# Kernel optimization log

Hardware: AMD Instinct MI355X
Metric: run time of the kernel (lower is better)

## Reference

```python
import jax, jax.numpy as jnp
import numpy as np

B, T, D, S, EXP = 4, 2048, 1024, 16, 2
E = D * EXP  # expanded channels = 2048


def setup_inputs() -> dict:
    key = jax.random.key(0)
    ks = jax.random.split(key, 8)
    s = 0.02
    f = jnp.float32
    return {
        "x": jax.random.normal(ks[0], (B, T, D), f),
        "in_w": jax.random.normal(ks[1], (2 * E, D), f) * s,
        "in_b": jnp.zeros((2 * E,), f),
        "conv_w": jax.random.normal(ks[2], (E, 1, 3), f) * s,  # depthwise conv, groups=E
        "conv_b": jnp.zeros((E,), f),
        "dt_w": jax.random.normal(ks[3], (E, E), f) * s,
        "dt_b": jnp.zeros((E,), f),
        "B_w": jax.random.normal(ks[4], (S, E), f) * s,
        "B_b": jnp.zeros((S,), f),
        "C_w": jax.random.normal(ks[5], (S, E), f) * s,
        "C_b": jnp.zeros((S,), f),
        "D_w": jax.random.normal(ks[6], (S, E), f) * s,
        "D_b": jnp.zeros((S,), f),
        "out_w": jax.random.normal(ks[7], (D, E), f) * s,
        "out_b": jnp.zeros((D,), f),
    }


def reference(x, in_w, in_b, conv_w, conv_b, dt_w, dt_b, B_w, B_b, C_w, C_b, D_w, D_b, out_w, out_b):
    silu = jax.nn.silu
    # in_proj -> split into main / gate, each [B,T,E]
    xp = x @ in_w.T + in_b
    x_main, x_gate = xp[..., :E], xp[..., E:]
    # depthwise temporal conv (kernel 3, pad 1, groups=E), then SiLU
    xc = jax.lax.conv_general_dilated(
        x_main.transpose(0, 2, 1), conv_w, (1,), [(1, 1)],
        dimension_numbers=("NCH", "OIH", "NCH"), feature_group_count=E)
    xc = silu((xc + conv_b[None, :, None]).transpose(0, 2, 1))  # [B,T,E]
    dt = jax.nn.softplus(xc @ dt_w.T + dt_b)                     # [B,T,E]
    Bt = xc @ B_w.T + B_b                                        # [B,T,S]
    Ct = xc @ C_w.T + C_b
    Dt = xc @ D_w.T + D_b
    decay = jnp.exp(jnp.clip(-dt.mean(-1), -10.0, 10.0))         # [B,T] scalar decay per step
    u = Bt * Dt                                                  # [B,T,S] state input

    def step(state, inp):  # state [B,S]
        d, u_t, c_t = inp
        state = state * d[:, None] + u_t
        return state, (c_t * state).sum(-1)  # y_t [B]

    _, ys = jax.lax.scan(step, jnp.zeros((x.shape[0], S), x.dtype),
                         (decay.T, u.transpose(1, 0, 2), Ct.transpose(1, 0, 2)))
    y = ys.T[..., None] * silu(x_gate)  # broadcast [B,T,1] -> [B,T,E] (matches .expand)
    return x + (y @ out_w.T + out_b)    # dropout in eval mode = identity
```

## Files before the change

kernel.cpp:

```cpp
#include <hip/hip_runtime.h>
#include <hip/hip_bf16.h>

#define Bsz 4
#define Tsz 2048
#define Dsz 1024
#define Ssz 16
#define Esz 2048
#define Mrows (Bsz*Tsz)

typedef __attribute__((ext_vector_type(8))) short short8;
typedef __attribute__((ext_vector_type(4))) float floatx4;
typedef __attribute__((ext_vector_type(8))) int int8v;
typedef __attribute__((ext_vector_type(4))) int int4v;

__device__ __forceinline__ void async_ld16(const void* g, void* l) {
    __builtin_amdgcn_global_load_lds(
        (const __attribute__((address_space(1))) void*)g,
        (__attribute__((address_space(3))) void*)l,
        16, 0, 0);
}

__device__ __forceinline__ float sigmoidf_(float v) { return 1.f / (1.f + expf(-v)); }
__device__ __forceinline__ float bf2f(unsigned short u) {
    union { unsigned u32; float f; } c; c.u32 = (unsigned)u << 16; return c.f;
}
__device__ __forceinline__ int pk_fp8x4(float a, float b, float c, float d) {
    int lo = __builtin_amdgcn_cvt_pk_fp8_f32(a, b, 0, 0);
    int hi = __builtin_amdgcn_cvt_pk_fp8_f32(c, d, 0, 0);
    return (lo & 0xFFFF) | (hi << 16);
}

#define WAIT_VM(N)   (0xF70 | (N))

#define CV_S0 2097152
#define CV_S1 3145728
#define CV_S2 4194304
#define CV_S3 4718592
__global__ void cvt_all(const float4* __restrict__ x,  const float4* __restrict__ iw,
                        const float4* __restrict__ dw, const float4* __restrict__ ow,
                        int* __restrict__ x8, int* __restrict__ iw8,
                        int* __restrict__ dw8, int* __restrict__ ow8) {
    int i = blockIdx.x * blockDim.x + threadIdx.x;
    const int stride = gridDim.x * blockDim.x;
    for (; i < CV_S3; i += stride) {
        if (i < CV_S0) {
            float4 v = x[i];
            x8[i] = pk_fp8x4(v.x, v.y, v.z, v.w);
        } else if (i < CV_S1) {
            const int j = i - CV_S0;
            float4 v = iw[j];
            iw8[j] = pk_fp8x4(v.x * 64.f, v.y * 64.f, v.z * 64.f, v.w * 64.f);
        } else if (i < CV_S2) {
            const int j = i - CV_S1;
            float4 v = dw[j];
            dw8[j] = pk_fp8x4(v.x * 64.f, v.y * 64.f, v.z * 64.f, v.w * 64.f);
        } else {
            const int j = i - CV_S2;
            float4 v = ow[j];
            ow8[j] = pk_fp8x4(v.x * 64.f, v.y * 64.f, v.z * 64.f, v.w * 64.f);
        }
    }
}

template<int MODE, int SA, int SB>
__launch_bounds__(256, 2)
__global__ void gemm_f8(const unsigned char* __restrict__ A,
                        const unsigned char* __restrict__ Bw,
                        const float* __restrict__ bias,
                        int M, int N, int K,
                        __hip_bfloat16* __restrict__ outb,
                        float* __restrict__ rowsum,
                        const float* __restrict__ resid,
                        const float* __restrict__ ysv,
                        float* __restrict__ outf) {
    __shared__ __align__(16) unsigned char sA[2 * 16384];
    __shared__ __align__(16) unsigned char sB[2 * 16384];

    const int tid  = threadIdx.x;
    const int wave = tid >> 6, lane = tid & 63;
    const int wm = wave >> 1, wn = wave & 1;
    const int q = lane >> 4, lr = lane & 15;

    const int gx = gridDim.x, gy = gridDim.y;
    const int flat = blockIdx.y * gx + blockIdx.x;
    const int stripe = gy >> 3;
    const int xcd = flat & 7, local = flat >> 3;
    const int mt = xcd * stripe + (local % stripe);
    const int nt = local / stripe;
    const int m0 = mt * 128, n0 = nt * 128;

    floatx4 acc[4][4];
#pragma unroll
    for (int i = 0; i < 4; ++i)
#pragma unroll
        for (int j = 0; j < 4; ++j) acc[i][j] = (floatx4){0.f, 0.f, 0.f, 0.f};

    const unsigned char* pa[4];
    const unsigned char* pb[4];
#pragma unroll
    for (int i = 0; i < 4; ++i) {
        const int idx = i * 256 + tid, row = idx >> 3, s = idx & 7;
        pa[i] = A + (size_t)(m0 + row) * K + ((s ^ (row & 7)) * 16);
        pb[i] = Bw + (size_t)(n0 + row) * K + ((s ^ (row & 7)) * 16);
    }

    const int rA = wm * 64 + lr, rB = wn * 64 + lr;
    const int oA0 = rA * 128 + (((2 * q)     ^ (rA & 7)) * 16);
    const int oA1 = rA * 128 + (((2 * q + 1) ^ (rA & 7)) * 16);
    const int oB0 = rB * 128 + (((2 * q)     ^ (rB & 7)) * 16);
    const int oB1 = rB * 128 + (((2 * q + 1) ^ (rB & 7)) * 16);

#define F8_ISSUE(ST) do {                                                      \
        _Pragma("unroll")                                                      \
        for (int i = 0; i < 4; ++i) {                                          \
            async_ld16(pa[i], &sA[(ST) * 16384 + (i * 256 + wave * 64) * 16]); \
            pa[i] += 128;                                                      \
        }                                                                      \
        _Pragma("unroll")                                                      \
        for (int i = 0; i < 4; ++i) {                                          \
            async_ld16(pb[i], &sB[(ST) * 16384 + (i * 256 + wave * 64) * 16]); \
            pb[i] += 128;                                                      \
        }                                                                      \
    } while (0)

    const int ntiles = K >> 7;
    F8_ISSUE(0);
    for (int kt = 0; kt < ntiles; ++kt) {
        const int st = kt & 1;
        __builtin_amdgcn_s_waitcnt(WAIT_VM(0));
        __syncthreads();
        F8_ISSUE(st ^ 1);

        int8v a8[4], b8[4];
#pragma unroll
        for (int i = 0; i < 4; ++i) {
            int4v lo = *(const int4v*)&sA[st * 16384 + oA0 + i * 2048];
            int4v hi = *(const int4v*)&sA[st * 16384 + oA1 + i * 2048];
            a8[i] = __builtin_shufflevector(lo, hi, 0, 1, 2, 3, 4, 5, 6, 7);
        }
#pragma unroll
        for (int j = 0; j < 4; ++j) {
            int4v lo = *(const int4v*)&sB[st * 16384 + oB0 + j * 2048];
            int4v hi = *(const int4v*)&sB[st * 16384 + oB1 + j * 2048];
            b8[j] = __builtin_shufflevector(lo, hi, 0, 1, 2, 3, 4, 5, 6, 7);
        }
#pragma unroll
        for (int i = 0; i < 4; ++i)
#pragma unroll
            for (int j = 0; j < 4; ++j)
                acc[i][j] = __builtin_amdgcn_mfma_scale_f32_16x16x128_f8f6f4(
                    a8[i], b8[j], acc[i][j], 0, 0, 0, SA, 0, SB);
    }
#undef F8_ISSUE
    __builtin_amdgcn_s_waitcnt(WAIT_VM(0));

    if (MODE == 0) {
#pragma unroll
        for (int i = 0; i < 4; ++i) {
            const int row = m0 + wm * 64 + i * 16 + q * 4;
#pragma unroll
            for (int j = 0; j < 4; ++j) {
                const int col = n0 + wn * 64 + j * 16 + lr;
                const float bc = bias[col];
#pragma unroll
                for (int r = 0; r < 4; ++r)
                    outb[(size_t)(row + r) * N + col] = __float2bfloat16(acc[i][j][r] + bc);
            }
        }
    } else if (MODE == 1) {
#pragma unroll
        for (int i = 0; i < 4; ++i) {
            float rs[4] = {0.f, 0.f, 0.f, 0.f};
#pragma unroll
            for (int j = 0; j < 4; ++j) {
                const int col = n0 + wn * 64 + j * 16 + lr;
                const float bc = bias[col];
#pragma unroll
                for (int r = 0; r < 4; ++r) {
                    float v = acc[i][j][r] + bc;
                    float sp = (v > 20.f) ? v : log1pf(expf(v));
                    rs[r] += sp;
                }
            }
#pragma unroll
            for (int r = 0; r < 4; ++r) {
                float v = rs[r];
                v += __shfl_xor(v, 1); v += __shfl_xor(v, 2);
                v += __shfl_xor(v, 4); v += __shfl_xor(v, 8);
                if (lr == 0)
                    atomicAdd(&rowsum[m0 + wm * 64 + i * 16 + q * 4 + r], v);
            }
        }
    } else {
#pragma unroll
        for (int i = 0; i < 4; ++i) {
            const int row = m0 + wm * 64 + i * 16 + q * 4;
#pragma unroll
            for (int j = 0; j < 4; ++j) {
                const int col = n0 + wn * 64 + j * 16 + lr;
                const float bc = bias[col];
#pragma unroll
                for (int r = 0; r < 4; ++r) {
                    const size_t idx = (size_t)(row + r) * N + col;
                    outf[idx] = resid[idx] + ysv[row + r] * acc[i][j][r] + bc;
                }
            }
        }
    }
}

__global__ void conv_gate_k(const __hip_bfloat16* __restrict__ xp,
                            const float* __restrict__ cw,
                            const float* __restrict__ cb,
                            __hip_bfloat16* __restrict__ xc,
                            int2* __restrict__ xc8,
                            int2* __restrict__ s8) {
    const int idx8 = blockIdx.x * blockDim.x + threadIdx.x;
    const int e = (idx8 & (Esz / 8 - 1)) * 8;
    const int r = idx8 >> 8;
    const int t = r & (Tsz - 1);
    const unsigned short* row0 = (const unsigned short*)(xp + (size_t)r * (2 * Esz) + e);
    short8 vm1 = (t > 0)       ? *(const short8*)(row0 - 2 * Esz) : (short8){0,0,0,0,0,0,0,0};
    short8 v00 = *(const short8*)row0;
    short8 vp1 = (t < Tsz - 1) ? *(const short8*)(row0 + 2 * Esz) : (short8){0,0,0,0,0,0,0,0};
    short8 o;
    float sil[8];
#pragma unroll
    for (int k = 0; k < 8; ++k) {
        const int ek = e + k;
        float v = bf2f((unsigned short)vm1[k]) * cw[ek * 3 + 0]
                + bf2f((unsigned short)v00[k]) * cw[ek * 3 + 1]
                + bf2f((unsigned short)vp1[k]) * cw[ek * 3 + 2] + cb[ek];
        sil[k] = v * sigmoidf_(v);
        __hip_bfloat16 h = __float2bfloat16(sil[k]);
        o[k] = *(short*)&h;
    }
    *(short8*)(xc + (size_t)idx8 * 8) = o;
    int2 p;
    p.x = pk_fp8x4(sil[0] * 16.f, sil[1] * 16.f, sil[2] * 16.f, sil[3] * 16.f);
    p.y = pk_fp8x4(sil[4] * 16.f, sil[5] * 16.f, sil[6] * 16.f, sil[7] * 16.f);
    xc8[idx8] = p;

    short8 g = *(const short8*)(row0 + Esz);
    float sg[8];
#pragma unroll
    for (int k = 0; k < 8; ++k) {
        const float gv = bf2f((unsigned short)g[k]);
        sg[k] = gv * sigmoidf_(gv);
    }
    int2 ps;
    ps.x = pk_fp8x4(sg[0] * 16.f, sg[1] * 16.f, sg[2] * 16.f, sg[3] * 16.f);
    ps.y = pk_fp8x4(sg[4] * 16.f, sg[5] * 16.f, sg[6] * 16.f, sg[7] * 16.f);
    s8[idx8] = ps;
}

__global__ void pack_bcd(const float* __restrict__ Bw, const float* __restrict__ Cw,
                         const float* __restrict__ Dw, __hip_bfloat16* __restrict__ Wb) {
    const int idx = blockIdx.x * blockDim.x + threadIdx.x;
    if (idx >= 48 * Esz) return;
    const int row = idx >> 11, col = idx & (Esz - 1);
    float v;
    if (row < 16)      v = Bw[row * Esz + col];
    else if (row < 32) v = Cw[(row - 16) * Esz + col];
    else               v = Dw[(row - 32) * Esz + col];
    Wb[idx] = __float2bfloat16(v);
}

__launch_bounds__(256)
__global__ void bcd_mfma(const __hip_bfloat16* __restrict__ xc,
                         const __hip_bfloat16* __restrict__ Wb,
                         const float* __restrict__ Bb, const float* __restrict__ Cb,
                         const float* __restrict__ Db,
                         float* __restrict__ u, float* __restrict__ Ct) {
    __shared__ __align__(16) __hip_bfloat16 sA[64 * 32];
    __shared__ __align__(16) __hip_bfloat16 sW[48 * 32];
    const int tid = threadIdx.x;
    const int wave = tid >> 6, lane = tid & 63;
    const int q = lane >> 4, lr = lane & 15;
    const int m0 = blockIdx.x * 64;

    floatx4 acc[3];
#pragma unroll
    for (int j = 0; j < 3; ++j) acc[j] = (floatx4){0.f, 0.f, 0.f, 0.f};

    const int ra = wave * 16 + (lane >> 2);
    const int ca = (lane & 3) * 8;

    for (int kt = 0; kt < (Esz >> 5); ++kt) {
        const int k0 = kt << 5;
        __syncthreads();
        async_ld16(&xc[(size_t)(m0 + ra) * Esz + k0 + ca], &sA[wave * 512]);
        if (wave < 3)
            async_ld16(&Wb[(size_t)ra * Esz + k0 + ca], &sW[wave * 512]);
        __syncthreads();

        short8 af = *(const short8*)&sA[(wave * 16 + lr) * 32 + q * 8];
#pragma unroll
        for (int j = 0; j < 3; ++j) {
            short8 wf = *(const short8*)&sW[(j * 16 + lr) * 32 + q * 8];
            acc[j] = __builtin_amdgcn_mfma_f32_16x16x32_bf16(af, wf, acc[j], 0, 0, 0);
        }
    }

    const int row = m0 + wave * 16 + q * 4;
    const float bb = Bb[lr], cbv = Cb[lr], db = Db[lr];
#pragma unroll
    for (int r = 0; r < 4; ++r) {
        const float bt = acc[0][r] + bb;
        const float ct = acc[1][r] + cbv;
        const float dt = acc[2][r] + db;
        u [(size_t)(row + r) * Ssz + lr] = bt * dt;
        Ct[(size_t)(row + r) * Ssz + lr] = ct;
    }
}

__global__ void scan_k(const float* __restrict__ rowsum, const float* __restrict__ u,
                       const float* __restrict__ Ct, float* __restrict__ ys) {
    const int b = blockIdx.x;
    const int tid = threadIdx.x;
    const int lane = tid & 63, wave = tid >> 6;
    __shared__ __align__(16) float su[256 * Ssz];
    __shared__ __align__(16) float sc[256 * Ssz];
    __shared__ float sp[256 * 17];
    __shared__ float sd[256];
    float st = 0.f;
    for (int t0 = 0; t0 < Tsz; t0 += 256) {
        __syncthreads();
        const float4* ub = (const float4*)(u  + ((size_t)b * Tsz + t0) * Ssz);
        const float4* cb = (const float4*)(Ct + ((size_t)b * Tsz + t0) * Ssz);
#pragma unroll
        for (int i = 0; i < 4; ++i) {
            ((float4*)su)[tid + i * 256] = ub[tid + i * 256];
            ((float4*)sc)[tid + i * 256] = cb[tid + i * 256];
        }
        {
            const float m = rowsum[b * Tsz + t0 + tid] * (1.f / (float)Esz);
            sd[tid] = expf(fminf(fmaxf(-m, -10.f), 10.f));
        }
        __syncthreads();
        if (wave == 0 && lane < 16) {
#pragma unroll 8
            for (int i = 0; i < 256; ++i) {
                st = st * sd[i] + su[i * Ssz + lane];
                sp[i * 17 + lane] = sc[i * Ssz + lane] * st;
            }
        }
        __syncthreads();
        float s = 0.f;
#pragma unroll
        for (int j = 0; j < 16; ++j) s += sp[tid * 17 + j];
        ys[b * Tsz + t0 + tid] = s;
    }
}

extern "C" void kernel_launch(void* const* d_in, const int* in_sizes, int n_in,
                              void* d_out, int out_size, void* d_ws, size_t ws_size,
                              hipStream_t stream) {
    const float* x      = (const float*)d_in[0];
    const float* in_w   = (const float*)d_in[1];
    const float* in_b   = (const float*)d_in[2];
    const float* conv_w = (const float*)d_in[3];
    const float* conv_b = (const float*)d_in[4];
    const float* dt_w   = (const float*)d_in[5];
    const float* dt_b   = (const float*)d_in[6];
    const float* B_w    = (const float*)d_in[7];
    const float* B_b    = (const float*)d_in[8];
    const float* C_w    = (const float*)d_in[9];
    const float* C_b    = (const float*)d_in[10];
    const float* D_w    = (const float*)d_in[11];
    const float* D_b    = (const float*)d_in[12];
    const float* out_w  = (const float*)d_in[13];
    const float* out_b  = (const float*)d_in[14];
    float* out = (float*)d_out;

    char* ws = (char*)d_ws;
    auto alloc = [&](size_t bytes) {
        char* p = ws;
        ws += (bytes + 255) & ~(size_t)255;
        return p;
    };
    unsigned char* x_f8    = (unsigned char*)alloc((size_t)Mrows * Dsz);
    unsigned char* inw_f8  = (unsigned char*)alloc((size_t)2 * Esz * Dsz);
    unsigned char* dtw_f8  = (unsigned char*)alloc((size_t)Esz * Esz);
    unsigned char* outw_f8 = (unsigned char*)alloc((size_t)Dsz * Esz);
    __hip_bfloat16* xp_bf  = (__hip_bfloat16*)alloc((size_t)Mrows * 2 * Esz * 2);
    __hip_bfloat16* xc_bf  = (__hip_bfloat16*)alloc((size_t)Mrows * Esz * 2);
    unsigned char* xc_f8   = (unsigned char*)alloc((size_t)Mrows * Esz);
    unsigned char* s_f8    = (unsigned char*)alloc((size_t)Mrows * Esz);
    __hip_bfloat16* wb_bf  = (__hip_bfloat16*)alloc((size_t)48 * Esz * 2);
    float* rowsum = (float*)alloc(Mrows * 4);
    float* u_buf  = (float*)alloc((size_t)Mrows * Ssz * 4);
    float* ct_buf = (float*)alloc((size_t)Mrows * Ssz * 4);
    float* ys_buf = (float*)alloc(Mrows * 4);
    (void)alloc(65536);

    hipMemsetAsync(rowsum, 0, Mrows * 4, stream);

    cvt_all<<<4608, 256, 0, stream>>>((const float4*)x, (const float4*)in_w,
                                      (const float4*)dt_w, (const float4*)out_w,
                                      (int*)x_f8, (int*)inw_f8, (int*)dtw_f8,
                                      (int*)outw_f8);
    pack_bcd<<<48 * Esz / 256, 256, 0, stream>>>(B_w, C_w, D_w, wb_bf);

    gemm_f8<0, 127, 121><<<dim3(4096 / 128, Mrows / 128), 256, 0, stream>>>(
        x_f8, inw_f8, in_b, Mrows, 4096, 1024, xp_bf, nullptr, nullptr, nullptr, nullptr);

    conv_gate_k<<<(Mrows * Esz / 8) / 256, 256, 0, stream>>>(
        xp_bf, conv_w, conv_b, xc_bf, (int2*)xc_f8, (int2*)s_f8);

    gemm_f8<1, 123, 121><<<dim3(Esz / 128, Mrows / 128), 256, 0, stream>>>(
        xc_f8, dtw_f8, dt_b, Mrows, Esz, Esz, nullptr, rowsum, nullptr, nullptr, nullptr);

    bcd_mfma<<<Mrows / 64, 256, 0, stream>>>(xc_bf, wb_bf, B_b, C_b, D_b, u_buf, ct_buf);

    scan_k<<<Bsz, 256, 0, stream>>>(rowsum, u_buf, ct_buf, ys_buf);

    gemm_f8<2, 123, 121><<<dim3(Dsz / 128, Mrows / 128), 256, 0, stream>>>(
        s_f8, outw_f8, out_b, Mrows, Dsz, Esz, nullptr, nullptr, x, ys_buf, out);
}
```

Baseline: 442.3 us.

## Use 256x256 tile FP8 GEMM with split-phase prefetch for in_proj and dt GEMMs

Adds a 512-thread GEMM kernel with 256x256 output tiles, 8 waves, and compile-time K/N for the in_proj and dt projections. Its K loop interleaves the async global-to-LDS loads of the next tile with the MFMA work, using partial waitcnts, split barriers and s_setprio. The larger tile is meant to raise arithmetic intensity and cut global and L2 traffic per flop. The cost is 128KB of LDS per block, more accumulator registers, and fewer blocks than compute units (512 and 256), which risks poor occupancy and tail imbalance. The out_proj GEMM stays on the 128x128 kernel.

```diff
diff --git a/kernel.cpp b/kernel.cpp
--- a/kernel.cpp
+++ b/kernel.cpp
@@ -62,17 +62,189 @@
     }
 }
 
-template<int MODE, int SA, int SB>
-__launch_bounds__(256, 2)
-__global__ void gemm_f8(const unsigned char* __restrict__ A,
+template<int MODE, int SA, int SB, int K, int N>
+__launch_bounds__(512, 2)
+__global__ void gemm256(const unsigned char* __restrict__ A,
                         const unsigned char* __restrict__ Bw,
                         const float* __restrict__ bias,
-                        int M, int N, int K,
                         __hip_bfloat16* __restrict__ outb,
-                        float* __restrict__ rowsum,
-                        const float* __restrict__ resid,
-                        const float* __restrict__ ysv,
-                        float* __restrict__ outf) {
+                        float* __restrict__ rowsum) {
+    __shared__ __align__(16) unsigned char sA[2 * 32768];
+    __shared__ __align__(16) unsigned char sB[2 * 32768];
+
+    const int tid  = threadIdx.x;
+    const int wave = tid >> 6, lane = tid & 63;
+    const int wm = wave >> 2, wn = wave & 3;
+    const int q = lane >> 4, lr = lane & 15;
+
+    const int gx = gridDim.x;
+    const int flat = blockIdx.y * gx + blockIdx.x;
+    const int xcd = flat & 7, local = flat >> 3;
+    const int mt = xcd * 4 + (local & 3);
+    const int nt = local >> 2;
+    const int m0 = mt * 256, n0 = nt * 256;
+
+    floatx4 acc[8][4];
+#pragma unroll
+    for (int i = 0; i < 8; ++i)
+#pragma unroll
+        for (int j = 0; j < 4; ++j) acc[i][j] = (floatx4){0.f, 0.f, 0.f, 0.f};
+
+    const int rowin = lane >> 3;
+    const int chunk = (lane & 7) ^ rowin;
+    const unsigned char* pa = A  + (size_t)(m0 + wave * 8 + rowin) * K + chunk * 16;
+    const unsigned char* pb = Bw + (size_t)(n0 + wave * 8 + rowin) * K + chunk * 16;
+    const int ldsw = wave * 8 * 128;
+
+    const int c0 = ((2 * q)     ^ (lr & 7)) * 16;
+    const int c1 = ((2 * q + 1) ^ (lr & 7)) * 16;
+    const int oA = (wm * 128 + lr) * 128;
+    const int oB = (wn * 64  + lr) * 128;
+
+#define G256_ISSUE_B(r) async_ld16(pb + (size_t)(r) * 64 * K + koff, \
+                                   &sB[sbo + ((r) * 64 * 128) + ldsw])
+#define G256_ISSUE_A(r) async_ld16(pa + (size_t)(r) * 64 * K + koff, \
+                                   &sA[sbo + ((r) * 64 * 128) + ldsw])
+#define G256_RD(dst, base, off) do {                                        \
+        int4v lo_ = *(const int4v*)&(base)[(off) + c0];                     \
+        int4v hi_ = *(const int4v*)&(base)[(off) + c1];                     \
+        dst = __builtin_shufflevector(lo_, hi_, 0, 1, 2, 3, 4, 5, 6, 7);    \
+    } while (0)
+
+    {
+        const size_t koff = 0; const int sbo = 0;
+        G256_ISSUE_B(0); G256_ISSUE_B(1); G256_ISSUE_B(2); G256_ISSUE_B(3);
+        G256_ISSUE_A(0); G256_ISSUE_A(2); G256_ISSUE_A(1); G256_ISSUE_A(3);
+    }
+
+    const int NT = K >> 7;
+    for (int kt = 0; kt < NT; ++kt) {
+        const int sb  = (kt & 1) * 32768;
+        const int sbo = ((kt + 1) & 1) * 32768;
+        const size_t koff = (size_t)(kt + 1) * 128;
+
+        __builtin_amdgcn_s_waitcnt(WAIT_VM(2));
+        __builtin_amdgcn_s_barrier();
+        G256_ISSUE_B(0); G256_ISSUE_B(1);
+        int8v b8[4];
+#pragma unroll
+        for (int g = 0; g < 4; ++g) G256_RD(b8[g], &sB[sb], oB + g * 2048);
+        {
+            int8v a0, a1;
+            G256_RD(a0, &sA[sb], oA + 0 * 2048);
+            G256_RD(a1, &sA[sb], oA + 1 * 2048);
+            __builtin_amdgcn_s_setprio(1);
+#pragma unroll
+            for (int g = 0; g < 4; ++g) {
+                acc[0][g] = __builtin_amdgcn_mfma_scale_f32_16x16x128_f8f6f4(
+                    a0, b8[g], acc[0][g], 0, 0, 0, SA, 0, SB);
+                acc[1][g] = __builtin_amdgcn_mfma_scale_f32_16x16x128_f8f6f4(
+                    a1, b8[g], acc[1][g], 0, 0, 0, SA, 0, SB);
+            }
+            __builtin_amdgcn_s_setprio(0);
+        }
+        G256_ISSUE_B(2); G256_ISSUE_B(3);
+        {
+            int8v a0, a1;
+            G256_RD(a0, &sA[sb], oA + 2 * 2048);
+            G256_RD(a1, &sA[sb], oA + 3 * 2048);
+            __builtin_amdgcn_s_setprio(1);
+#pragma unroll
+            for (int g = 0; g < 4; ++g) {
+                acc[2][g] = __builtin_amdgcn_mfma_scale_f32_16x16x128_f8f6f4(
+                    a0, b8[g], acc[2][g], 0, 0, 0, SA, 0, SB);
+                acc[3][g] = __builtin_amdgcn_mfma_scale_f32_16x16x128_f8f6f4(
+                    a1, b8[g], acc[3][g], 0, 0, 0, SA, 0, SB);
+            }
+            __builtin_amdgcn_s_setprio(0);
+        }
+        __builtin_amdgcn_s_waitcnt(WAIT_VM(4));
+        __builtin_amdgcn_s_barrier();
+        G256_ISSUE_A(0); G256_ISSUE_A(2);
+        {
+            int8v a0, a1;
+            G256_RD(a0, &sA[sb], oA + 4 * 2048);
+            G256_RD(a1, &sA[sb], oA + 5 * 2048);
+            __builtin_amdgcn_s_setprio(1);
+#pragma unroll
+            for (int g = 0; g < 4; ++g) {
+                acc[4][g] = __builtin_amdgcn_mfma_scale_f32_16x16x128_f8f6f4(
+                    a0, b8[g], acc[4][g], 0, 0, 0, SA, 0, SB);
+                acc[5][g] = __builtin_amdgcn_mfma_scale_f32_16x16x128_f8f6f4(
+                    a1, b8[g], acc[5][g], 0, 0, 0, SA, 0, SB);
+            }
+            __builtin_amdgcn_s_setprio(0);
+        }
+        G256_ISSUE_A(1); G256_ISSUE_A(3);
+        {
+            int8v a0, a1;
+            G256_RD(a0, &sA[sb], oA + 6 * 2048);
+            G256_RD(a1, &sA[sb], oA + 7 * 2048);
+            __builtin_amdgcn_s_setprio(1);
+#pragma unroll
+            for (int g = 0; g < 4; ++g) {
+                acc[6][g] = __builtin_amdgcn_mfma_scale_f32_16x16x128_f8f6f4(
+                    a0, b8[g], acc[6][g], 0, 0, 0, SA, 0, SB);
+                acc[7][g] = __builtin_amdgcn_mfma_scale_f32_16x16x128_f8f6f4(
+                    a1, b8[g], acc[7][g], 0, 0, 0, SA, 0, SB);
+            }
+            __builtin_amdgcn_s_setprio(0);
+        }
+    }
+#undef G256_ISSUE_B
+#undef G256_ISSUE_A
+#undef G256_RD
+    __builtin_amdgcn_s_waitcnt(WAIT_VM(0));
+
+    if (MODE == 0) {
+#pragma unroll
+        for (int i = 0; i < 8; ++i) {
+            const int row = m0 + wm * 128 + i * 16 + q * 4;
+#pragma unroll
+            for (int j = 0; j < 4; ++j) {
+                const int col = n0 + wn * 64 + j * 16 + lr;
+                const float bc = bias[col];
+#pragma unroll
+                for (int r = 0; r < 4; ++r)
+                    outb[(size_t)(row + r) * N + col] = __float2bfloat16(acc[i][j][r] + bc);
+            }
+        }
+    } else {
+#pragma unroll
+        for (int i = 0; i < 8; ++i) {
+            float rs[4] = {0.f, 0.f, 0.f, 0.f};
+#pragma unroll
+            for (int j = 0; j < 4; ++j) {
+                const int col = n0 + wn * 64 + j * 16 + lr;
+                const float bc = bias[col];
+#pragma unroll
+                for (int r = 0; r < 4; ++r) {
+                    float v = acc[i][j][r] + bc;
+                    float sp = (v > 20.f) ? v : log1pf(expf(v));
+                    rs[r] += sp;
+                }
+            }
+#pragma unroll
+            for (int r = 0; r < 4; ++r) {
+                float v = rs[r];
+                v += __shfl_xor(v, 1); v += __shfl_xor(v, 2);
+                v += __shfl_xor(v, 4); v += __shfl_xor(v, 8);
+                if (lr == 0)
+                    atomicAdd(&rowsum[m0 + wm * 128 + i * 16 + q * 4 + r], v);
+            }
+        }
+    }
+}
+
+template<int SA, int SB>
+__launch_bounds__(256, 2)
+__global__ void gemm_f8_sm(const unsigned char* __restrict__ A,
+                           const unsigned char* __restrict__ Bw,
+                           const float* __restrict__ bias,
+                           int M, int N, int K,
+                           const float* __restrict__ resid,
+                           const float* __restrict__ ysv,
+                           float* __restrict__ outf) {
     __shared__ __align__(16) unsigned char sA[2 * 16384];
     __shared__ __align__(16) unsigned char sB[2 * 16384];
 
@@ -123,9 +295,9 @@
         }                                                                      \
     } while (0)
 
-    const int ntiles = K >> 7;
+    const int ntile = K >> 7;
     F8_ISSUE(0);
-    for (int kt = 0; kt < ntiles; ++kt) {
+    for (int kt = 0; kt < ntile; ++kt) {
         const int st = kt & 1;
         __builtin_amdgcn_s_waitcnt(WAIT_VM(0));
         __syncthreads();
@@ -154,56 +326,17 @@
 #undef F8_ISSUE
     __builtin_amdgcn_s_waitcnt(WAIT_VM(0));
 
-    if (MODE == 0) {
-#pragma unroll
-        for (int i = 0; i < 4; ++i) {
-            const int row = m0 + wm * 64 + i * 16 + q * 4;
-#pragma unroll
-            for (int j = 0; j < 4; ++j) {
-                const int col = n0 + wn * 64 + j * 16 + lr;
-                const float bc = bias[col];
-#pragma unroll
-                for (int r = 0; r < 4; ++r)
-                    outb[(size_t)(row + r) * N + col] = __float2bfloat16(acc[i][j][r] + bc);
-            }
-        }
-    } else if (MODE == 1) {
-#pragma unroll
-        for (int i = 0; i < 4; ++i) {
-            float rs[4] = {0.f, 0.f, 0.f, 0.f};
-#pragma unroll
-            for (int j = 0; j < 4; ++j) {
-                const int col = n0 + wn * 64 + j * 16 + lr;
-                const float bc = bias[col];
-#pragma unroll
-                for (int r = 0; r < 4; ++r) {
-                    float v = acc[i][j][r] + bc;
-                    float sp = (v > 20.f) ? v : log1pf(expf(v));
-                    rs[r] += sp;
-                }
-            }
+#pragma unroll
+    for (int i = 0; i < 4; ++i) {
+        const int row = m0 + wm * 64 + i * 16 + q * 4;
+#pragma unroll
+        for (int j = 0; j < 4; ++j) {
+            const int col = n0 + wn * 64 + j * 16 + lr;
+            const float bc = bias[col];
 #pragma unroll
             for (int r = 0; r < 4; ++r) {
-                float v = rs[r];
-                v += __shfl_xor(v, 1); v += __shfl_xor(v, 2);
-                v += __shfl_xor(v, 4); v += __shfl_xor(v, 8);
-                if (lr == 0)
-                    atomicAdd(&rowsum[m0 + wm * 64 + i * 16 + q * 4 + r], v);
-            }
-        }
-    } else {
-#pragma unroll
-        for (int i = 0; i < 4; ++i) {
-            const int row = m0 + wm * 64 + i * 16 + q * 4;
-#pragma unroll
-            for (int j = 0; j < 4; ++j) {
-                const int col = n0 + wn * 64 + j * 16 + lr;
-                const float bc = bias[col];
-#pragma unroll
-                for (int r = 0; r < 4; ++r) {
-                    const size_t idx = (size_t)(row + r) * N + col;
-                    outf[idx] = resid[idx] + ysv[row + r] * acc[i][j][r] + bc;
-                }
+                const size_t idx = (size_t)(row + r) * N + col;
+                outf[idx] = resid[idx] + ysv[row + r] * acc[i][j][r] + bc;
             }
         }
     }
@@ -392,7 +525,7 @@
     float* u_buf  = (float*)alloc((size_t)Mrows * Ssz * 4);
     float* ct_buf = (float*)alloc((size_t)Mrows * Ssz * 4);
     float* ys_buf = (float*)alloc(Mrows * 4);
-    (void)alloc(65536);
+    (void)alloc(131072);
 
     hipMemsetAsync(rowsum, 0, Mrows * 4, stream);
 
@@ -402,19 +535,19 @@
                                       (int*)outw_f8);
     pack_bcd<<<48 * Esz / 256, 256, 0, stream>>>(B_w, C_w, D_w, wb_bf);
 
-    gemm_f8<0, 127, 121><<<dim3(4096 / 128, Mrows / 128), 256, 0, stream>>>(
-        x_f8, inw_f8, in_b, Mrows, 4096, 1024, xp_bf, nullptr, nullptr, nullptr, nullptr);
+    gemm256<0, 127, 121, 1024, 4096><<<dim3(16, 32), 512, 0, stream>>>(
+        x_f8, inw_f8, in_b, xp_bf, nullptr);
 
     conv_gate_k<<<(Mrows * Esz / 8) / 256, 256, 0, stream>>>(
         xp_bf, conv_w, conv_b, xc_bf, (int2*)xc_f8, (int2*)s_f8);
 
-    gemm_f8<1, 123, 121><<<dim3(Esz / 128, Mrows / 128), 256, 0, stream>>>(
-        xc_f8, dtw_f8, dt_b, Mrows, Esz, Esz, nullptr, rowsum, nullptr, nullptr, nullptr);
+    gemm256<1, 123, 121, 2048, 2048><<<dim3(8, 32), 512, 0, stream>>>(
+        xc_f8, dtw_f8, dt_b, nullptr, rowsum);
 
     bcd_mfma<<<Mrows / 64, 256, 0, stream>>>(xc_bf, wb_bf, B_b, C_b, D_b, u_buf, ct_buf);
 
     scan_k<<<Bsz, 256, 0, stream>>>(rowsum, u_buf, ct_buf, ys_buf);
 
-    gemm_f8<2, 123, 121><<<dim3(Dsz / 128, Mrows / 128), 256, 0, stream>>>(
-        s_f8, outw_f8, out_b, Mrows, Dsz, Esz, nullptr, nullptr, x, ys_buf, out);
-}
+    gemm_f8_sm<123, 121><<<dim3(Dsz / 128, Mrows / 128), 256, 0, stream>>>(
+        s_f8, outw_f8, out_b, Mrows, Dsz, Esz, x, ys_buf, out);
+}
```

New measurement: 447.4 us. About the same (+1.2%).

## Switch GEMM pipeline from scaled FP8 MFMA to BF16 MFMA

Applied to the files above, without the earlier changes.

Replaces the FP8 scaled 16x16x128 MFMA GEMMs with BF16 16x16x32 MFMA GEMMs, converting inputs, weights and the conv/gate activations to bf16 instead of fp8. K tiles shrink to 32 elements with 8 KB LDS stages, the XOR swizzle is dropped, and launch bounds rise to 3 blocks per CU. This likely aims at accuracy or simplicity, but it doubles the bytes moved and quarters the K per MFMA. It also risks LDS bank conflicts from the unswizzled layout.

```diff
diff --git a/kernel.cpp b/kernel.cpp
--- a/kernel.cpp
+++ b/kernel.cpp
@@ -10,8 +10,7 @@
 
 typedef __attribute__((ext_vector_type(8))) short short8;
 typedef __attribute__((ext_vector_type(4))) float floatx4;
-typedef __attribute__((ext_vector_type(8))) int int8v;
-typedef __attribute__((ext_vector_type(4))) int int4v;
+typedef __attribute__((ext_vector_type(4))) unsigned short ushort4v;
 
 __device__ __forceinline__ void async_ld16(const void* g, void* l) {
     __builtin_amdgcn_global_load_lds(
@@ -24,10 +23,9 @@
 __device__ __forceinline__ float bf2f(unsigned short u) {
     union { unsigned u32; float f; } c; c.u32 = (unsigned)u << 16; return c.f;
 }
-__device__ __forceinline__ int pk_fp8x4(float a, float b, float c, float d) {
-    int lo = __builtin_amdgcn_cvt_pk_fp8_f32(a, b, 0, 0);
-    int hi = __builtin_amdgcn_cvt_pk_fp8_f32(c, d, 0, 0);
-    return (lo & 0xFFFF) | (hi << 16);
+__device__ __forceinline__ unsigned short f2bf(float f) {
+    __hip_bfloat16 h = __float2bfloat16(f);
+    return *(unsigned short*)&h;
 }
 
 #define WAIT_VM(N)   (0xF70 | (N))
@@ -38,33 +36,25 @@
 #define CV_S3 4718592
 __global__ void cvt_all(const float4* __restrict__ x,  const float4* __restrict__ iw,
                         const float4* __restrict__ dw, const float4* __restrict__ ow,
-                        int* __restrict__ x8, int* __restrict__ iw8,
-                        int* __restrict__ dw8, int* __restrict__ ow8) {
+                        ushort4v* __restrict__ xb, ushort4v* __restrict__ iwb,
+                        ushort4v* __restrict__ dwb, ushort4v* __restrict__ owb) {
     int i = blockIdx.x * blockDim.x + threadIdx.x;
     const int stride = gridDim.x * blockDim.x;
     for (; i < CV_S3; i += stride) {
-        if (i < CV_S0) {
-            float4 v = x[i];
-            x8[i] = pk_fp8x4(v.x, v.y, v.z, v.w);
-        } else if (i < CV_S1) {
-            const int j = i - CV_S0;
-            float4 v = iw[j];
-            iw8[j] = pk_fp8x4(v.x * 64.f, v.y * 64.f, v.z * 64.f, v.w * 64.f);
-        } else if (i < CV_S2) {
-            const int j = i - CV_S1;
-            float4 v = dw[j];
-            dw8[j] = pk_fp8x4(v.x * 64.f, v.y * 64.f, v.z * 64.f, v.w * 64.f);
-        } else {
-            const int j = i - CV_S2;
-            float4 v = ow[j];
-            ow8[j] = pk_fp8x4(v.x * 64.f, v.y * 64.f, v.z * 64.f, v.w * 64.f);
-        }
-    }
-}
-
-template<int MODE, int SA, int SB>
-__launch_bounds__(256, 2)
-__global__ void gemm_f8(const unsigned char* __restrict__ A,
+        float4 v; ushort4v* dst; int j;
+        if (i < CV_S0)      { j = i;         v = x[j];  dst = xb; }
+        else if (i < CV_S1) { j = i - CV_S0; v = iw[j]; dst = iwb; }
+        else if (i < CV_S2) { j = i - CV_S1; v = dw[j]; dst = dwb; }
+        else                { j = i - CV_S2; v = ow[j]; dst = owb; }
+        ushort4v o;
+        o[0] = f2bf(v.x); o[1] = f2bf(v.y); o[2] = f2bf(v.z); o[3] = f2bf(v.w);
+        dst[j] = o;
+    }
+}
+
+template<int MODE>
+__launch_bounds__(256, 3)
+__global__ void gemm_bf(const unsigned char* __restrict__ A,
                         const unsigned char* __restrict__ Bw,
                         const float* __restrict__ bias,
                         int M, int N, int K,
@@ -73,8 +63,8 @@
                         const float* __restrict__ resid,
                         const float* __restrict__ ysv,
                         float* __restrict__ outf) {
-    __shared__ __align__(16) unsigned char sA[2 * 16384];
-    __shared__ __align__(16) unsigned char sB[2 * 16384];
+    __shared__ __align__(16) unsigned char sA[2 * 8192];
+    __shared__ __align__(16) unsigned char sB[2 * 8192];
 
     const int tid  = threadIdx.x;
     const int wave = tid >> 6, lane = tid & 63;
@@ -95,63 +85,56 @@
 #pragma unroll
         for (int j = 0; j < 4; ++j) acc[i][j] = (floatx4){0.f, 0.f, 0.f, 0.f};
 
-    const unsigned char* pa[4];
-    const unsigned char* pb[4];
-#pragma unroll
-    for (int i = 0; i < 4; ++i) {
-        const int idx = i * 256 + tid, row = idx >> 3, s = idx & 7;
-        pa[i] = A + (size_t)(m0 + row) * K + ((s ^ (row & 7)) * 16);
-        pb[i] = Bw + (size_t)(n0 + row) * K + ((s ^ (row & 7)) * 16);
-    }
-
-    const int rA = wm * 64 + lr, rB = wn * 64 + lr;
-    const int oA0 = rA * 128 + (((2 * q)     ^ (rA & 7)) * 16);
-    const int oA1 = rA * 128 + (((2 * q + 1) ^ (rA & 7)) * 16);
-    const int oB0 = rB * 128 + (((2 * q)     ^ (rB & 7)) * 16);
-    const int oB1 = rB * 128 + (((2 * q + 1) ^ (rB & 7)) * 16);
-
-#define F8_ISSUE(ST) do {                                                      \
+    const size_t rbytes = (size_t)K * 2;
+    const unsigned char* pa[2];
+    const unsigned char* pb[2];
+#pragma unroll
+    for (int i = 0; i < 2; ++i) {
+        const int idx = i * 256 + tid, row = idx >> 2, ch = idx & 3;
+        pa[i] = A  + (size_t)(m0 + row) * rbytes + ch * 16;
+        pb[i] = Bw + (size_t)(n0 + row) * rbytes + ch * 16;
+    }
+
+    const int oA = (wm * 64 + lr) * 64 + q * 16;
+    const int oB = (wn * 64 + lr) * 64 + q * 16;
+
+#define BF_ISSUE(ST) do {                                                      \
         _Pragma("unroll")                                                      \
-        for (int i = 0; i < 4; ++i) {                                          \
-            async_ld16(pa[i], &sA[(ST) * 16384 + (i * 256 + wave * 64) * 16]); \
-            pa[i] += 128;                                                      \
+        for (int i = 0; i < 2; ++i) {                                          \
+            async_ld16(pa[i], &sA[(ST) * 8192 + (i * 256 + wave * 64) * 16]);  \
+            pa[i] += 64;                                                       \
         }                                                                      \
         _Pragma("unroll")                                                      \
-        for (int i = 0; i < 4; ++i) {                                          \
-            async_ld16(pb[i], &sB[(ST) * 16384 + (i * 256 + wave * 64) * 16]); \
-            pb[i] += 128;                                                      \
+        for (int i = 0; i < 2; ++i) {                                          \
+            async_ld16(pb[i], &sB[(ST) * 8192 + (i * 256 + wave * 64) * 16]);  \
+            pb[i] += 64;                                                       \
         }                                                                      \
     } while (0)
 
-    const int ntiles = K >> 7;
-    F8_ISSUE(0);
-    for (int kt = 0; kt < ntiles; ++kt) {
+    const int ntile = K >> 5;
+    BF_ISSUE(0);
+    for (int kt = 0; kt < ntile; ++kt) {
         const int st = kt & 1;
+        const int base = st * 8192;
         __builtin_amdgcn_s_waitcnt(WAIT_VM(0));
         __syncthreads();
-        F8_ISSUE(st ^ 1);
-
-        int8v a8[4], b8[4];
-#pragma unroll
-        for (int i = 0; i < 4; ++i) {
-            int4v lo = *(const int4v*)&sA[st * 16384 + oA0 + i * 2048];
-            int4v hi = *(const int4v*)&sA[st * 16384 + oA1 + i * 2048];
-            a8[i] = __builtin_shufflevector(lo, hi, 0, 1, 2, 3, 4, 5, 6, 7);
-        }
-#pragma unroll
-        for (int j = 0; j < 4; ++j) {
-            int4v lo = *(const int4v*)&sB[st * 16384 + oB0 + j * 2048];
-            int4v hi = *(const int4v*)&sB[st * 16384 + oB1 + j * 2048];
-            b8[j] = __builtin_shufflevector(lo, hi, 0, 1, 2, 3, 4, 5, 6, 7);
-        }
+        BF_ISSUE(st ^ 1);
+
+        short8 a8[4], b8[4];
 #pragma unroll
         for (int i = 0; i < 4; ++i)
+            a8[i] = *(const short8*)&sA[base + oA + i * 1024];
+#pragma unroll
+        for (int j = 0; j < 4; ++j)
+            b8[j] = *(const short8*)&sB[base + oB + j * 1024];
+#pragma unroll
+        for (int i = 0; i < 4; ++i)
 #pragma unroll
             for (int j = 0; j < 4; ++j)
-                acc[i][j] = __builtin_amdgcn_mfma_scale_f32_16x16x128_f8f6f4(
-                    a8[i], b8[j], acc[i][j], 0, 0, 0, SA, 0, SB);
-    }
-#undef F8_ISSUE
+                acc[i][j] = __builtin_amdgcn_mfma_f32_16x16x32_bf16(
+                    a8[i], b8[j], acc[i][j], 0, 0, 0);
+    }
+#undef BF_ISSUE
     __builtin_amdgcn_s_waitcnt(WAIT_VM(0));
 
     if (MODE == 0) {
@@ -213,8 +196,7 @@
                             const float* __restrict__ cw,
                             const float* __restrict__ cb,
                             __hip_bfloat16* __restrict__ xc,
-                            int2* __restrict__ xc8,
-                            int2* __restrict__ s8) {
+                            __hip_bfloat16* __restrict__ sgate) {
     const int idx8 = blockIdx.x * blockDim.x + threadIdx.x;
     const int e = (idx8 & (Esz / 8 - 1)) * 8;
     const int r = idx8 >> 8;
@@ -224,34 +206,25 @@
     short8 v00 = *(const short8*)row0;
     short8 vp1 = (t < Tsz - 1) ? *(const short8*)(row0 + 2 * Esz) : (short8){0,0,0,0,0,0,0,0};
     short8 o;
-    float sil[8];
 #pragma unroll
     for (int k = 0; k < 8; ++k) {
         const int ek = e + k;
         float v = bf2f((unsigned short)vm1[k]) * cw[ek * 3 + 0]
                 + bf2f((unsigned short)v00[k]) * cw[ek * 3 + 1]
                 + bf2f((unsigned short)vp1[k]) * cw[ek * 3 + 2] + cb[ek];
-        sil[k] = v * sigmoidf_(v);
-        __hip_bfloat16 h = __float2bfloat16(sil[k]);
-        o[k] = *(short*)&h;
+        float sil = v * sigmoidf_(v);
+        o[k] = (short)f2bf(sil);
     }
     *(short8*)(xc + (size_t)idx8 * 8) = o;
-    int2 p;
-    p.x = pk_fp8x4(sil[0] * 16.f, sil[1] * 16.f, sil[2] * 16.f, sil[3] * 16.f);
-    p.y = pk_fp8x4(sil[4] * 16.f, sil[5] * 16.f, sil[6] * 16.f, sil[7] * 16.f);
-    xc8[idx8] = p;
 
     short8 g = *(const short8*)(row0 + Esz);
-    float sg[8];
+    short8 os;
 #pragma unroll
     for (int k = 0; k < 8; ++k) {
         const float gv = bf2f((unsigned short)g[k]);
-        sg[k] = gv * sigmoidf_(gv);
-    }
-    int2 ps;
-    ps.x = pk_fp8x4(sg[0] * 16.f, sg[1] * 16.f, sg[2] * 16.f, sg[3] * 16.f);
-    ps.y = pk_fp8x4(sg[4] * 16.f, sg[5] * 16.f, sg[6] * 16.f, sg[7] * 16.f);
-    s8[idx8] = ps;
+        os[k] = (short)f2bf(gv * sigmoidf_(gv));
+    }
+    *(short8*)(sgate + (size_t)idx8 * 8) = os;
 }
 
 __global__ void pack_bcd(const float* __restrict__ Bw, const float* __restrict__ Cw,
@@ -379,42 +352,44 @@
         ws += (bytes + 255) & ~(size_t)255;
         return p;
     };
-    unsigned char* x_f8    = (unsigned char*)alloc((size_t)Mrows * Dsz);
-    unsigned char* inw_f8  = (unsigned char*)alloc((size_t)2 * Esz * Dsz);
-    unsigned char* dtw_f8  = (unsigned char*)alloc((size_t)Esz * Esz);
-    unsigned char* outw_f8 = (unsigned char*)alloc((size_t)Dsz * Esz);
+    __hip_bfloat16* x_bf   = (__hip_bfloat16*)alloc((size_t)Mrows * Dsz * 2);
+    __hip_bfloat16* inw_bf = (__hip_bfloat16*)alloc((size_t)2 * Esz * Dsz * 2);
+    __hip_bfloat16* dtw_bf = (__hip_bfloat16*)alloc((size_t)Esz * Esz * 2);
+    __hip_bfloat16* outw_bf= (__hip_bfloat16*)alloc((size_t)Dsz * Esz * 2);
     __hip_bfloat16* xp_bf  = (__hip_bfloat16*)alloc((size_t)Mrows * 2 * Esz * 2);
     __hip_bfloat16* xc_bf  = (__hip_bfloat16*)alloc((size_t)Mrows * Esz * 2);
-    unsigned char* xc_f8   = (unsigned char*)alloc((size_t)Mrows * Esz);
-    unsigned char* s_f8    = (unsigned char*)alloc((size_t)Mrows * Esz);
+    __hip_bfloat16* s_bf   = (__hip_bfloat16*)alloc((size_t)Mrows * Esz * 2);
     __hip_bfloat16* wb_bf  = (__hip_bfloat16*)alloc((size_t)48 * Esz * 2);
     float* rowsum = (float*)alloc(Mrows * 4);
     float* u_buf  = (float*)alloc((size_t)Mrows * Ssz * 4);
     float* ct_buf = (float*)alloc((size_t)Mrows * Ssz * 4);
     float* ys_buf = (float*)alloc(Mrows * 4);
-    (void)alloc(65536);
+    (void)alloc(131072);
 
     hipMemsetAsync(rowsum, 0, Mrows * 4, stream);
 
     cvt_all<<<4608, 256, 0, stream>>>((const float4*)x, (const float4*)in_w,
                                       (const float4*)dt_w, (const float4*)out_w,
-                                      (int*)x_f8, (int*)inw_f8, (int*)dtw_f8,
-                                      (int*)outw_f8);
+                                      (ushort4v*)x_bf, (ushort4v*)inw_bf,
+                                      (ushort4v*)dtw_bf, (ushort4v*)outw_bf);
     pack_bcd<<<48 * Esz / 256, 256, 0, stream>>>(B_w, C_w, D_w, wb_bf);
 
-    gemm_f8<0, 127, 121><<<dim3(4096 / 128, Mrows / 128), 256, 0, stream>>>(
-        x_f8, inw_f8, in_b, Mrows, 4096, 1024, xp_bf, nullptr, nullptr, nullptr, nullptr);
+    gemm_bf<0><<<dim3(4096 / 128, Mrows / 128), 256, 0, stream>>>(
+        (const unsigned char*)x_bf, (const unsigned char*)inw_bf, in_b,
+        Mrows, 4096, 1024, xp_bf, nullptr, nullptr, nullptr, nullptr);
 
     conv_gate_k<<<(Mrows * Esz / 8) / 256, 256, 0, stream>>>(
-        xp_bf, conv_w, conv_b, xc_bf, (int2*)xc_f8, (int2*)s_f8);
-
-    gemm_f8<1, 123, 121><<<dim3(Esz / 128, Mrows / 128), 256, 0, stream>>>(
-        xc_f8, dtw_f8, dt_b, Mrows, Esz, Esz, nullptr, rowsum, nullptr, nullptr, nullptr);
+        xp_bf, conv_w, conv_b, xc_bf, s_bf);
+
+    gemm_bf<1><<<dim3(Esz / 128, Mrows / 128), 256, 0, stream>>>(
+        (const unsigned char*)xc_bf, (const unsigned char*)dtw_bf, dt_b,
+        Mrows, Esz, Esz, nullptr, rowsum, nullptr, nullptr, nullptr);
 
     bcd_mfma<<<Mrows / 64, 256, 0, stream>>>(xc_bf, wb_bf, B_b, C_b, D_b, u_buf, ct_buf);
 
     scan_k<<<Bsz, 256, 0, stream>>>(rowsum, u_buf, ct_buf, ys_buf);
 
-    gemm_f8<2, 123, 121><<<dim3(Dsz / 128, Mrows / 128), 256, 0, stream>>>(
-        s_f8, outw_f8, out_b, Mrows, Dsz, Esz, nullptr, nullptr, x, ys_buf, out);
-}
+    gemm_bf<2><<<dim3(Dsz / 128, Mrows / 128), 256, 0, stream>>>(
+        (const unsigned char*)s_bf, (const unsigned char*)outw_bf, out_b,
+        Mrows, Dsz, Esz, nullptr, nullptr, x, ys_buf, out);
+}
```

Result: slower. 511.6 us (+15.7%).
